# Optimization experiments

Measured on AMD Instinct MI355X. Metric: run time of the kernel, lower is better.

The kernel has to match this reference:

```python
import jax, jax.numpy as jnp
import numpy as np

DIM = 384
DIM_HEAD = 32
HEADS = DIM // DIM_HEAD  # 12
WIN = 8
DIM_FF = 1536
FUSED = DIM + DIM + DIM_FF  # 2304


def setup_inputs() -> dict:
    key = jax.random.key(0)
    ks = jax.random.split(key, 8)
    B, H, W = 16, 64, 64
    x = jax.random.normal(ks[0], (B, DIM, H, W), dtype=jnp.float32)
    s = lambda fan_in: 1.0 / np.sqrt(fan_in)
    w_fused = jax.random.normal(ks[1], (FUSED, DIM), dtype=jnp.float32) * s(DIM)
    w_gate = jax.random.normal(ks[2], (HEADS, DIM), dtype=jnp.float32) * s(DIM)
    b_gate = jnp.full((HEADS,), 0.5, dtype=jnp.float32)  # init_constant_(0.5)
    w_attn_out = jax.random.normal(ks[3], (DIM, DIM), dtype=jnp.float32) * s(DIM)
    w_ff_out = jax.random.normal(ks[4], (DIM, DIM_FF), dtype=jnp.float32) * s(DIM_FF)
    # StarReLU learnable scalars (metaformer defaults)
    sr_scale = jnp.asarray(0.8944, dtype=jnp.float32)
    sr_bias = jnp.asarray(-0.4472, dtype=jnp.float32)
    return {"x": x, "w_fused": w_fused, "w_gate": w_gate, "b_gate": b_gate,
            "w_attn_out": w_attn_out, "w_ff_out": w_ff_out,
            "sr_scale": sr_scale, "sr_bias": sr_bias}


def reference(x, w_fused, w_gate, b_gate, w_attn_out, w_ff_out, sr_scale, sr_bias):
    B, C, H, W = x.shape
    p = WIN
    gh, gw = H // p, W // p
    n = p * p
    # b c (h p1) (w p2) -> (b h w) (p1 p2) c
    xw = x.reshape(B, C, gh, p, gw, p).transpose(0, 2, 4, 3, 5, 1).reshape(B * gh * gw, n, C)
    fused = jnp.einsum('bnc,fc->bnf', xw, w_fused)  # [Bw, n, 2304]
    q, kv, x_ff = jnp.split(fused, [DIM, 2 * DIM], axis=-1)
    # b n (h d) -> b h n d
    q = q.reshape(-1, n, HEADS, DIM_HEAD).transpose(0, 2, 1, 3)
    kv = kv.reshape(-1, n, HEADS, DIM_HEAD).transpose(0, 2, 1, 3)
    scale = 1.0 / np.sqrt(DIM_HEAD)
    scores = jnp.einsum('bhnd,bhmd->bhnm', q, kv) * scale
    attn = jax.nn.softmax(scores, axis=-1)
    x_attn = jnp.einsum('bhnm,bhmd->bhnd', attn, kv)  # kv is both key and value
    gate = jnp.einsum('bnc,hc->bnh', xw, w_gate) + b_gate  # [Bw, n, heads]
    x_attn = x_attn * jax.nn.sigmoid(gate.transpose(0, 2, 1)[..., None])
    x_attn = x_attn.transpose(0, 2, 1, 3).reshape(-1, n, DIM)
    ff = sr_scale * jnp.square(jax.nn.relu(x_ff)) + sr_bias  # StarReLU
    out = jnp.einsum('bnc,oc->bno', x_attn, w_attn_out) + jnp.einsum('bnf,of->bno', ff, w_ff_out)
    # (b h w) (p1 p2) c -> b c (h p1) (w p2)
    out = out.reshape(B, gh, gw, p, p, C).transpose(0, 5, 1, 3, 2, 4).reshape(B, C, H, W)
    return out
```

## Files before the change

### kernel.cpp

```cpp
#include <hip/hip_runtime.h>
#include <hip/hip_bf16.h>

typedef __bf16 bf16x8 __attribute__((ext_vector_type(8), may_alias));
typedef float f32x4 __attribute__((ext_vector_type(4), may_alias));
typedef unsigned short ushort_a __attribute__((may_alias));
typedef unsigned int uint_a __attribute__((may_alias));
typedef unsigned short us8 __attribute__((ext_vector_type(8), may_alias));

#define MFMA(a, b, c) __builtin_amdgcn_mfma_f32_16x16x32_bf16(a, b, c, 0, 0, 0)

__device__ __forceinline__ unsigned short f2bf(float f) {
  return __builtin_bit_cast(unsigned short, (__bf16)f);
}
__device__ __forceinline__ float bf2f(unsigned short u) {
  unsigned v = ((unsigned)u) << 16;
  return __builtin_bit_cast(float, v);
}

__device__ __forceinline__ void kbar() {
  __builtin_amdgcn_sched_barrier(0);
  asm volatile("s_waitcnt lgkmcnt(0)" ::: "memory");
  __builtin_amdgcn_sched_barrier(0);
  __builtin_amdgcn_s_barrier();
  __builtin_amdgcn_sched_barrier(0);
}

#define OFF_WG 884736
#define OFF_WAO 933888
#define OFF_WFO 1081344
#define OFF_XG 1671168
#define OFF_FUSED 26836992
#define OFF_GATE 177831936

__global__ __launch_bounds__(256) void prep_weights(
    const float* __restrict__ wf, const float* __restrict__ wg,
    const float* __restrict__ wao, const float* __restrict__ wfo,
    unsigned short* __restrict__ ws) {
  int i = blockIdx.x * 256 + threadIdx.x;
  if (i < 884736) { ws[i] = f2bf(wf[i]); return; }
  int j = i - 884736;
  if (j < 49152) { ws[i] = f2bf(j < 4608 ? wg[j] : 0.0f); return; }
  j -= 49152;
  if (j < 147456) { ws[i] = f2bf(wao[j]); return; }
  j -= 147456;
  if (j < 589824) ws[i] = f2bf(wfo[j]);
}

__global__ __launch_bounds__(256) void k0_gather(const float* __restrict__ x,
                                                 unsigned short* __restrict__ xg) {
  __shared__ __align__(16) char As[49152];
  int tid = threadIdx.x, wi = blockIdx.x;
  int b = wi >> 6, ghi = (wi >> 3) & 7, gwi = wi & 7;
  const float* xb = x + (size_t)b * 1572864 + (ghi * 8) * 64 + gwi * 8;
  for (int it = 0; it < 12; ++it) {
    int idx = it * 256 + tid;
    int c = idx % 384, p1 = idx / 384;
    const float* src = xb + (size_t)c * 4096 + p1 * 64;
    float4 v0 = *(const float4*)src, v1 = *(const float4*)(src + 4);
    float f[8] = {v0.x, v0.y, v0.z, v0.w, v1.x, v1.y, v1.z, v1.w};
#pragma unroll
    for (int jj = 0; jj < 8; ++jj) {
      int row = p1 * 8 + jj;
      int byte = (row * 768 + c * 2) ^ ((row & 7) << 4);
      *(ushort_a*)(As + byte) = f2bf(f[jj]);
    }
  }
  __syncthreads();
  unsigned short* og = xg + (size_t)wi * 24576;
#pragma unroll
  for (int it = 0; it < 12; ++it) {
    int idx = it * 256 + tid;
    int row = idx / 48, c = idx % 48;
    int byte = (row * 768 + c * 16) ^ ((row & 7) << 4);
    *(us8*)(og + (size_t)row * 384 + c * 8) = *(us8*)(As + byte);
  }
}

__global__ __launch_bounds__(512, 4) void k1_gemm(unsigned short* __restrict__ ws,
                                                  const float* __restrict__ srs,
                                                  const float* __restrict__ srb) {
  __shared__ __align__(16) char sm[65536];
  const int tid = threadIdx.x, lane = tid & 63, wave = tid >> 6;
  const int l15 = lane & 15, l4 = lane >> 4;
  const int wr = wave & 3, wc = wave >> 2;
  const int bid = blockIdx.x;
  const int swz = (bid & 7) * 1216 + (bid >> 3);
  const int mb = swz / 19, nb = swz - mb * 19;
  const unsigned short* Ab = ws + OFF_XG + (size_t)mb * 128 * 384;
  const unsigned short* Bb =
      (nb < 18) ? ws + (size_t)nb * 128 * 384 : ws + OFF_WG;
  const int srow = tid >> 3, sc = tid & 7;
  f32x4 of[2][4] = {};
  us8 sA0[2], sB0[2], sA1[2], sB1[2];

#define K1_LOAD(KS, SA, SB)                                                   \
  {                                                                           \
    _Pragma("unroll") for (int r2 = 0; r2 < 2; ++r2) {                        \
      int row = srow + 64 * r2;                                               \
      SA[r2] = *(const us8*)(Ab + (size_t)row * 384 + (KS)*64 + sc * 8);      \
      SB[r2] = *(const us8*)(Bb + (size_t)row * 384 + (KS)*64 + sc * 8);      \
    }                                                                         \
  }
#define K1_WRITE(BUF, SA, SB)                                                 \
  {                                                                           \
    _Pragma("unroll") for (int r2 = 0; r2 < 2; ++r2) {                        \
      int row = srow + 64 * r2;                                               \
      int byte = ((row * 128 + sc * 16) ^ ((row & 7) << 4)) + (BUF);          \
      *(us8*)(sm + byte) = SA[r2];                                            \
      *(us8*)(sm + 32768 + byte) = SB[r2];                                    \
    }                                                                         \
  }
#define K1_COMPUTE(BUF)                                                       \
  {                                                                           \
    _Pragma("unroll") for (int kk = 0; kk < 2; ++kk) {                        \
      bf16x8 af[2], bfr[4];                                                   \
      _Pragma("unroll") for (int mt = 0; mt < 2; ++mt) {                      \
        int row = wr * 32 + mt * 16 + l15;                                    \
        af[mt] = *(const bf16x8*)(sm + (BUF) +                                \
                 ((row * 128 + kk * 64 + l4 * 16) ^ ((row & 7) << 4)));       \
      }                                                                       \
      _Pragma("unroll") for (int nt = 0; nt < 4; ++nt) {                      \
        int row = wc * 64 + nt * 16 + l15;                                    \
        bfr[nt] = *(const bf16x8*)(sm + 32768 + (BUF) +                       \
                  ((row * 128 + kk * 64 + l4 * 16) ^ ((row & 7) << 4)));      \
      }                                                                       \
      _Pragma("unroll") for (int mt = 0; mt < 2; ++mt)                        \
      _Pragma("unroll") for (int nt = 0; nt < 4; ++nt)                        \
          of[mt][nt] = MFMA(af[mt], bfr[nt], of[mt][nt]);                     \
    }                                                                         \
  }

  K1_LOAD(0, sA0, sB0);
  K1_LOAD(1, sA1, sB1);
  K1_WRITE(0, sA0, sB0);
  __syncthreads();
#pragma unroll 1
  for (int kp = 0; kp < 3; ++kp) {
    int ks = kp * 2;
    if (ks + 2 < 6) K1_LOAD(ks + 2, sA0, sB0);
    K1_COMPUTE(0);
    K1_WRITE(16384, sA1, sB1);
    kbar();
    if (ks + 3 < 6) K1_LOAD(ks + 3, sA1, sB1);
    K1_COMPUTE(16384);
    if (ks + 2 < 6) K1_WRITE(0, sA0, sB0);
    kbar();
  }
  const float ssc = srs[0], sbi = srb[0];
  const bool ffreg = (nb >= 6) && (nb < 18);
#pragma unroll
  for (int mt = 0; mt < 2; ++mt)
#pragma unroll
    for (int nt = 0; nt < 4; ++nt)
#pragma unroll
      for (int rr = 0; rr < 4; ++rr) {
        int row = wr * 32 + mt * 16 + l4 * 4 + rr;
        int col = wc * 64 + nt * 16 + l15;
        float v = of[mt][nt][rr];
        if (ffreg) { v = fmaxf(v, 0.0f); v = ssc * v * v + sbi; }
        *(ushort_a*)(sm + ((row * 256 + col * 2) ^ ((row & 7) << 4))) = f2bf(v);
      }
  __syncthreads();
  if (nb < 18) {
    unsigned short* fo = ws + OFF_FUSED + (size_t)mb * 128 * 2304 + nb * 128;
#pragma unroll
    for (int r2 = 0; r2 < 4; ++r2) {
      int idx = r2 * 512 + tid;
      int row = idx >> 4, c = idx & 15;
      int byte = (row * 256 + c * 16) ^ ((row & 7) << 4);
      __builtin_nontemporal_store(*(us8*)(sm + byte),
                                  (us8*)(fo + (size_t)row * 2304 + c * 8));
    }
  } else {
    unsigned short* go = ws + OFF_GATE + (size_t)mb * 128 * 16;
#pragma unroll
    for (int r2 = 0; r2 < 4; ++r2) {
      int idx = r2 * 512 + tid;
      int row = idx >> 4, c = idx & 15;
      if (c < 2) {
        int byte = (row * 256 + c * 16) ^ ((row & 7) << 4);
        __builtin_nontemporal_store(*(us8*)(sm + byte),
                                    (us8*)(go + (size_t)row * 16 + c * 8));
      }
    }
  }
}

__global__ __launch_bounds__(256, 3) void k2_attn(unsigned short* __restrict__ ws,
                                                  const float* __restrict__ bgate) {
  __shared__ __align__(16) char sm[49152];
  const int tid = threadIdx.x, lane = tid & 63, wave = tid >> 6;
  const int l15 = lane & 15, l4 = lane >> 4;
  char* kvT = sm + wave * 12288;
  char* Pb = kvT + 4096;
  const int wi = blockIdx.x;
  const size_t T0 = (size_t)wi * 64;
  unsigned short* fused = ws + OFF_FUSED;
  const unsigned short* gb = ws + OFF_GATE;
  const f32x4 zz = {};
#pragma unroll 1
  for (int hi = 0; hi < 3; ++hi) {
    const int h = wave + hi * 4;
    bf16x8 akv[4], bq[4];
#pragma unroll
    for (int t = 0; t < 4; ++t) {
      akv[t] = *(const bf16x8*)(fused + (T0 + t * 16 + l15) * 2304 + 384 + h * 32 + l4 * 8);
      bq[t] = *(const bf16x8*)(fused + (T0 + t * 16 + l15) * 2304 + h * 32 + l4 * 8);
    }
    f32x4 sfT[4][4];
#pragma unroll
    for (int mt = 0; mt < 4; ++mt)
#pragma unroll
      for (int ni = 0; ni < 4; ++ni) sfT[mt][ni] = MFMA(akv[mt], bq[ni], zz);
#pragma unroll
    for (int mt = 0; mt < 4; ++mt) {
      us8 u = __builtin_bit_cast(us8, akv[mt]);
      int m = mt * 16 + l15;
#pragma unroll
      for (int j = 0; j < 8; ++j) {
        int d = l4 * 8 + j;
        *(ushort_a*)(kvT + ((d * 128 + m * 2) ^ ((d & 7) << 4))) = u[j];
      }
    }
#pragma unroll
    for (int ni = 0; ni < 4; ++ni) {
      float s[16];
#pragma unroll
      for (int mt = 0; mt < 4; ++mt)
#pragma unroll
        for (int rr = 0; rr < 4; ++rr)
          s[mt * 4 + rr] = sfT[mt][ni][rr] * 0.176776695f;
      float mx = s[0];
#pragma unroll
      for (int q2 = 1; q2 < 16; ++q2) mx = fmaxf(mx, s[q2]);
      mx = fmaxf(mx, __shfl_xor(mx, 16, 64));
      mx = fmaxf(mx, __shfl_xor(mx, 32, 64));
      float sum = 0.0f;
#pragma unroll
      for (int q2 = 0; q2 < 16; ++q2) {
        s[q2] = __expf(s[q2] - mx);
        sum += s[q2];
      }
      sum += __shfl_xor(sum, 16, 64);
      sum += __shfl_xor(sum, 32, 64);
      float rs = 1.0f / sum;
      int n = ni * 16 + l15;
      int rowb = n * 128, sw = (n & 7) << 4;
#pragma unroll
      for (int mt = 0; mt < 4; ++mt) {
        int m = mt * 16 + l4 * 4;
        unsigned p0 = (unsigned)f2bf(s[mt * 4 + 0] * rs) |
                      ((unsigned)f2bf(s[mt * 4 + 1] * rs) << 16);
        unsigned p1 = (unsigned)f2bf(s[mt * 4 + 2] * rs) |
                      ((unsigned)f2bf(s[mt * 4 + 3] * rs) << 16);
        *(uint_a*)(Pb + ((rowb + m * 2) ^ sw)) = p0;
        *(uint_a*)(Pb + ((rowb + (m + 2) * 2) ^ sw)) = p1;
      }
    }
    f32x4 xo[4][2] = {};
#pragma unroll
    for (int ks = 0; ks < 2; ++ks) {
      bf16x8 bv[2];
#pragma unroll
      for (int dt = 0; dt < 2; ++dt) {
        int d = dt * 16 + l15;
        bv[dt] = *(const bf16x8*)(kvT + ((d * 128 + ks * 64 + l4 * 16) ^ ((d & 7) << 4)));
      }
#pragma unroll
      for (int nt = 0; nt < 4; ++nt) {
        int n = nt * 16 + l15;
        bf16x8 ap = *(const bf16x8*)(Pb + ((n * 128 + ks * 64 + l4 * 16) ^ ((n & 7) << 4)));
        xo[nt][0] = MFMA(ap, bv[0], xo[nt][0]);
        xo[nt][1] = MFMA(ap, bv[1], xo[nt][1]);
      }
    }
    const float bgh = bgate[h];
#pragma unroll
    for (int nt = 0; nt < 4; ++nt)
#pragma unroll
      for (int rr = 0; rr < 4; ++rr) {
        int n = nt * 16 + l4 * 4 + rr;
        float gv = bf2f(gb[(T0 + n) * 16 + h]) + bgh;
        float sg = 1.0f / (1.0f + __expf(-gv));
#pragma unroll
        for (int dt = 0; dt < 2; ++dt)
          fused[(T0 + n) * 2304 + h * 32 + dt * 16 + l15] =
              f2bf(xo[nt][dt][rr] * sg);
      }
  }
}

__global__ __launch_bounds__(512, 4) void k3_gemm(const unsigned short* __restrict__ ws,
                                                  float* __restrict__ out) {
  __shared__ __align__(16) char sm[65536];
  const int tid = threadIdx.x, lane = tid & 63, wave = tid >> 6;
  const int l15 = lane & 15, l4 = lane >> 4;
  const int wr = wave & 3, wc = wave >> 2;
  const int bid = blockIdx.x;
  const int swz = (bid & 7) * 192 + (bid >> 3);
  const int mb = swz / 3, nB = swz - mb * 3;
  const size_t T0 = (size_t)mb * 128;
  const unsigned short* fA = ws + OFF_FUSED + T0 * 2304;
  const unsigned short* wao = ws + OFF_WAO + (size_t)(nB * 128) * 384;
  const unsigned short* wfo = ws + OFF_WFO + (size_t)(nB * 128) * 1536;
  const int srow = tid >> 3, sc = tid & 7;
  f32x4 of[2][4] = {};
  us8 sA0[2], sB0[2], sA1[2], sB1[2];

#define K3_LOAD(KS, SA, SB)                                                   \
  {                                                                           \
    int ac = (KS) < 6 ? (KS)*64 : 768 + ((KS)-6) * 64;                        \
    _Pragma("unroll") for (int r2 = 0; r2 < 2; ++r2) {                        \
      int row = srow + 64 * r2;                                               \
      SA[r2] = *(const us8*)(fA + (size_t)row * 2304 + ac + sc * 8);          \
      if ((KS) < 6)                                                           \
        SB[r2] = *(const us8*)(wao + (size_t)row * 384 + (KS)*64 + sc * 8);   \
      else                                                                    \
        SB[r2] =                                                              \
            *(const us8*)(wfo + (size_t)row * 1536 + ((KS)-6) * 64 + sc * 8); \
    }                                                                         \
  }
#define K3_WRITE(BUF, SA, SB)                                                 \
  {                                                                           \
    _Pragma("unroll") for (int r2 = 0; r2 < 2; ++r2) {                        \
      int row = srow + 64 * r2;                                               \
      int byte = ((row * 128 + sc * 16) ^ ((row & 7) << 4)) + (BUF);          \
      *(us8*)(sm + byte) = SA[r2];                                            \
      *(us8*)(sm + 32768 + byte) = SB[r2];                                    \
    }                                                                         \
  }
#define K3_COMPUTE(BUF)                                                       \
  {                                                                           \
    _Pragma("unroll") for (int kk = 0; kk < 2; ++kk) {                        \
      bf16x8 af[2], bfr[4];                                                   \
      _Pragma("unroll") for (int mt = 0; mt < 2; ++mt) {                      \
        int row = wr * 32 + mt * 16 + l15;                                    \
        af[mt] = *(const bf16x8*)(sm + (BUF) +                                \
                 ((row * 128 + kk * 64 + l4 * 16) ^ ((row & 7) << 4)));       \
      }                                                                       \
      _Pragma("unroll") for (int nt = 0; nt < 4; ++nt) {                      \
        int row = wc * 64 + nt * 16 + l15;                                    \
        bfr[nt] = *(const bf16x8*)(sm + 32768 + (BUF) +                       \
                  ((row * 128 + kk * 64 + l4 * 16) ^ ((row & 7) << 4)));      \
      }                                                                       \
      _Pragma("unroll") for (int mt = 0; mt < 2; ++mt)                        \
      _Pragma("unroll") for (int nt = 0; nt < 4; ++nt)                        \
          of[mt][nt] = MFMA(af[mt], bfr[nt], of[mt][nt]);                     \
    }                                                                         \
  }

  K3_LOAD(0, sA0, sB0);
  K3_LOAD(1, sA1, sB1);
  K3_WRITE(0, sA0, sB0);
  __syncthreads();
#pragma unroll 1
  for (int kp = 0; kp < 15; ++kp) {
    int ks = kp * 2;
    if (ks + 2 < 30) K3_LOAD(ks + 2, sA0, sB0);
    K3_COMPUTE(0);
    K3_WRITE(16384, sA1, sB1);
    kbar();
    if (ks + 3 < 30) K3_LOAD(ks + 3, sA1, sB1);
    K3_COMPUTE(16384);
    if (ks + 2 < 30) K3_WRITE(0, sA0, sB0);
    kbar();
  }
#pragma unroll
  for (int mt = 0; mt < 2; ++mt) {
    int n0 = wr * 32 + mt * 16 + l4 * 4;
    int T = (int)T0 + n0;
    int wi = T >> 6, n = T & 63;
    int b = wi >> 6, ghi = (wi >> 3) & 7, gwi = wi & 7;
    float* ob = out + (size_t)b * 1572864 + (size_t)(ghi * 8 + (n >> 3)) * 64 +
                gwi * 8 + (n & 7);
#pragma unroll
    for (int nt = 0; nt < 4; ++nt) {
      int c = nB * 128 + wc * 64 + nt * 16 + l15;
      __builtin_nontemporal_store(of[mt][nt], (f32x4*)(ob + (size_t)c * 4096));
    }
  }
}

extern "C" void kernel_launch(void* const* d_in, const int* in_sizes, int n_in,
                              void* d_out, int out_size, void* d_ws, size_t ws_size,
                              hipStream_t stream) {
  const float* x = (const float*)d_in[0];
  const float* wf = (const float*)d_in[1];
  const float* wg = (const float*)d_in[2];
  const float* bg = (const float*)d_in[3];
  const float* wao = (const float*)d_in[4];
  const float* wfo = (const float*)d_in[5];
  const float* srs = (const float*)d_in[6];
  const float* srb = (const float*)d_in[7];
  unsigned short* ws = (unsigned short*)d_ws;

  prep_weights<<<6528, 256, 0, stream>>>(wf, wg, wao, wfo, ws);
  k0_gather<<<1024, 256, 0, stream>>>(x, ws + OFF_XG);
  k1_gemm<<<512 * 19, 512, 0, stream>>>(ws, srs, srb);
  k2_attn<<<1024, 256, 0, stream>>>(ws, bg);
  k3_gemm<<<512 * 3, 512, 0, stream>>>(ws, (float*)d_out);
}
```

Before: 478.4 us.

## Load GEMM A operand directly into registers, staging only B in LDS

In both the projection GEMM and the output GEMM, each wave now loads its A fragments straight from global memory in MFMA register layout, double-buffered in registers. Only the B tile still goes through swizzled LDS. This halves shared memory per block from 64KB to 32KB, which should allow more resident blocks and cuts LDS write and read traffic. The cost is that the two column-waves fetch the same A rows twice from cache, and those row-strided 16-byte loads are less coalesced than the old cooperative tile load.

```diff
diff --git a/kernel.cpp b/kernel.cpp
--- a/kernel.cpp
+++ b/kernel.cpp
@@ -79,7 +79,7 @@
 __global__ __launch_bounds__(512, 4) void k1_gemm(unsigned short* __restrict__ ws,
                                                   const float* __restrict__ srs,
                                                   const float* __restrict__ srb) {
-  __shared__ __align__(16) char sm[65536];
+  __shared__ __align__(16) char sm[32768];
   const int tid = threadIdx.x, lane = tid & 63, wave = tid >> 6;
   const int l15 = lane & 15, l4 = lane >> 4;
   const int wr = wave & 3, wc = wave >> 2;
@@ -90,60 +90,67 @@
   const unsigned short* Bb =
       (nb < 18) ? ws + (size_t)nb * 128 * 384 : ws + OFF_WG;
   const int srow = tid >> 3, sc = tid & 7;
+  const unsigned short* Arow0 = Ab + (size_t)(wr * 32 + l15) * 384 + l4 * 8;
+  const unsigned short* Arow1 = Arow0 + 16 * 384;
   f32x4 of[2][4] = {};
-  us8 sA0[2], sB0[2], sA1[2], sB1[2];
-
-#define K1_LOAD(KS, SA, SB)                                                   \
+  us8 sB0[2], sB1[2];
+  bf16x8 aA[4], aB[4];
+
+#define K1_LOADB(KS, SB)                                                      \
   {                                                                           \
     _Pragma("unroll") for (int r2 = 0; r2 < 2; ++r2) {                        \
       int row = srow + 64 * r2;                                               \
-      SA[r2] = *(const us8*)(Ab + (size_t)row * 384 + (KS)*64 + sc * 8);      \
       SB[r2] = *(const us8*)(Bb + (size_t)row * 384 + (KS)*64 + sc * 8);      \
     }                                                                         \
   }
-#define K1_WRITE(BUF, SA, SB)                                                 \
+#define K1_LOADA(KS, AR)                                                      \
+  {                                                                           \
+    AR[0] = *(const bf16x8*)(Arow0 + (KS)*64);                                \
+    AR[1] = *(const bf16x8*)(Arow0 + (KS)*64 + 32);                           \
+    AR[2] = *(const bf16x8*)(Arow1 + (KS)*64);                                \
+    AR[3] = *(const bf16x8*)(Arow1 + (KS)*64 + 32);                           \
+  }
+#define K1_WRITEB(BUF, SB)                                                    \
   {                                                                           \
     _Pragma("unroll") for (int r2 = 0; r2 < 2; ++r2) {                        \
       int row = srow + 64 * r2;                                               \
       int byte = ((row * 128 + sc * 16) ^ ((row & 7) << 4)) + (BUF);          \
-      *(us8*)(sm + byte) = SA[r2];                                            \
-      *(us8*)(sm + 32768 + byte) = SB[r2];                                    \
-    }                                                                         \
-  }
-#define K1_COMPUTE(BUF)                                                       \
+      *(us8*)(sm + byte) = SB[r2];                                            \
+    }                                                                         \
+  }
+#define K1_COMPUTE(BUF, AR)                                                   \
   {                                                                           \
     _Pragma("unroll") for (int kk = 0; kk < 2; ++kk) {                        \
-      bf16x8 af[2], bfr[4];                                                   \
-      _Pragma("unroll") for (int mt = 0; mt < 2; ++mt) {                      \
-        int row = wr * 32 + mt * 16 + l15;                                    \
-        af[mt] = *(const bf16x8*)(sm + (BUF) +                                \
-                 ((row * 128 + kk * 64 + l4 * 16) ^ ((row & 7) << 4)));       \
+      bf16x8 bfr[4];                                                          \
+      _Pragma("unroll") for (int nt = 0; nt < 4; ++nt) {                      \
+        int row = wc * 64 + nt * 16 + l15;                                    \
+        bfr[nt] = *(const bf16x8*)(sm + (BUF) +                               \
+                  ((row * 128 + kk * 64 + l4 * 16) ^ ((row & 7) << 4)));      \
       }                                                                       \
       _Pragma("unroll") for (int nt = 0; nt < 4; ++nt) {                      \
-        int row = wc * 64 + nt * 16 + l15;                                    \
-        bfr[nt] = *(const bf16x8*)(sm + 32768 + (BUF) +                       \
-                  ((row * 128 + kk * 64 + l4 * 16) ^ ((row & 7) << 4)));      \
+        of[0][nt] = MFMA(AR[kk], bfr[nt], of[0][nt]);                         \
+        of[1][nt] = MFMA(AR[2 + kk], bfr[nt], of[1][nt]);                     \
       }                                                                       \
-      _Pragma("unroll") for (int mt = 0; mt < 2; ++mt)                        \
-      _Pragma("unroll") for (int nt = 0; nt < 4; ++nt)                        \
-          of[mt][nt] = MFMA(af[mt], bfr[nt], of[mt][nt]);                     \
-    }                                                                         \
-  }
-
-  K1_LOAD(0, sA0, sB0);
-  K1_LOAD(1, sA1, sB1);
-  K1_WRITE(0, sA0, sB0);
+    }                                                                         \
+  }
+
+  K1_LOADB(0, sB0);
+  K1_LOADB(1, sB1);
+  K1_LOADA(0, aA);
+  K1_WRITEB(0, sB0);
   __syncthreads();
 #pragma unroll 1
   for (int kp = 0; kp < 3; ++kp) {
     int ks = kp * 2;
-    if (ks + 2 < 6) K1_LOAD(ks + 2, sA0, sB0);
-    K1_COMPUTE(0);
-    K1_WRITE(16384, sA1, sB1);
+    if (ks + 2 < 6) K1_LOADB(ks + 2, sB0);
+    K1_LOADA(ks + 1, aB);
+    K1_COMPUTE(0, aA);
+    K1_WRITEB(16384, sB1);
     kbar();
-    if (ks + 3 < 6) K1_LOAD(ks + 3, sA1, sB1);
-    K1_COMPUTE(16384);
-    if (ks + 2 < 6) K1_WRITE(0, sA0, sB0);
+    if (ks + 3 < 6) K1_LOADB(ks + 3, sB1);
+    if (ks + 2 < 6) K1_LOADA(ks + 2, aA);
+    K1_COMPUTE(16384, aB);
+    if (ks + 2 < 6) K1_WRITEB(0, sB0);
     kbar();
   }
   const float ssc = srs[0], sbi = srb[0];
@@ -292,7 +299,7 @@
 
 __global__ __launch_bounds__(512, 4) void k3_gemm(const unsigned short* __restrict__ ws,
                                                   float* __restrict__ out) {
-  __shared__ __align__(16) char sm[65536];
+  __shared__ __align__(16) char sm[32768];
   const int tid = threadIdx.x, lane = tid & 63, wave = tid >> 6;
   const int l15 = lane & 15, l4 = lane >> 4;
   const int wr = wave & 3, wc = wave >> 2;
@@ -304,15 +311,16 @@
   const unsigned short* wao = ws + OFF_WAO + (size_t)(nB * 128) * 384;
   const unsigned short* wfo = ws + OFF_WFO + (size_t)(nB * 128) * 1536;
   const int srow = tid >> 3, sc = tid & 7;
+  const unsigned short* Arow0 = fA + (size_t)(wr * 32 + l15) * 2304 + l4 * 8;
+  const unsigned short* Arow1 = Arow0 + 16 * 2304;
   f32x4 of[2][4] = {};
-  us8 sA0[2], sB0[2], sA1[2], sB1[2];
-
-#define K3_LOAD(KS, SA, SB)                                                   \
-  {                                                                           \
-    int ac = (KS) < 6 ? (KS)*64 : 768 + ((KS)-6) * 64;                        \
+  us8 sB0[2], sB1[2];
+  bf16x8 aA[4], aB[4];
+
+#define K3_LOADB(KS, SB)                                                      \
+  {                                                                           \
     _Pragma("unroll") for (int r2 = 0; r2 < 2; ++r2) {                        \
       int row = srow + 64 * r2;                                               \
-      SA[r2] = *(const us8*)(fA + (size_t)row * 2304 + ac + sc * 8);          \
       if ((KS) < 6)                                                           \
         SB[r2] = *(const us8*)(wao + (size_t)row * 384 + (KS)*64 + sc * 8);   \
       else                                                                    \
@@ -320,49 +328,55 @@
             *(const us8*)(wfo + (size_t)row * 1536 + ((KS)-6) * 64 + sc * 8); \
     }                                                                         \
   }
-#define K3_WRITE(BUF, SA, SB)                                                 \
+#define K3_LOADA(KS, AR)                                                      \
+  {                                                                           \
+    int ac = (KS) < 6 ? (KS)*64 : 768 + ((KS)-6) * 64;                        \
+    AR[0] = *(const bf16x8*)(Arow0 + ac);                                     \
+    AR[1] = *(const bf16x8*)(Arow0 + ac + 32);                                \
+    AR[2] = *(const bf16x8*)(Arow1 + ac);                                     \
+    AR[3] = *(const bf16x8*)(Arow1 + ac + 32);                                \
+  }
+#define K3_WRITEB(BUF, SB)                                                    \
   {                                                                           \
     _Pragma("unroll") for (int r2 = 0; r2 < 2; ++r2) {                        \
       int row = srow + 64 * r2;                                               \
       int byte = ((row * 128 + sc * 16) ^ ((row & 7) << 4)) + (BUF);          \
-      *(us8*)(sm + byte) = SA[r2];                                            \
-      *(us8*)(sm + 32768 + byte) = SB[r2];                                    \
-    }                                                                         \
-  }
-#define K3_COMPUTE(BUF)                                                       \
+      *(us8*)(sm + byte) = SB[r2];                                            \
+    }                                                                         \
+  }
+#define K3_COMPUTE(BUF, AR)                                                   \
   {                                                                           \
     _Pragma("unroll") for (int kk = 0; kk < 2; ++kk) {                        \
-      bf16x8 af[2], bfr[4];                                                   \
-      _Pragma("unroll") for (int mt = 0; mt < 2; ++mt) {                      \
-        int row = wr * 32 + mt * 16 + l15;                                    \
-        af[mt] = *(const bf16x8*)(sm + (BUF) +                                \
-                 ((row * 128 + kk * 64 + l4 * 16) ^ ((row & 7) << 4)));       \
+      bf16x8 bfr[4];                                                          \
+      _Pragma("unroll") for (int nt = 0; nt < 4; ++nt) {                      \
+        int row = wc * 64 + nt * 16 + l15;                                    \
+        bfr[nt] = *(const bf16x8*)(sm + (BUF) +                               \
+                  ((row * 128 + kk * 64 + l4 * 16) ^ ((row & 7) << 4)));      \
       }                                                                       \
       _Pragma("unroll") for (int nt = 0; nt < 4; ++nt) {                      \
-        int row = wc * 64 + nt * 16 + l15;                                    \
-        bfr[nt] = *(const bf16x8*)(sm + 32768 + (BUF) +                       \
-                  ((row * 128 + kk * 64 + l4 * 16) ^ ((row & 7) << 4)));      \
+        of[0][nt] = MFMA(AR[kk], bfr[nt], of[0][nt]);                         \
+        of[1][nt] = MFMA(AR[2 + kk], bfr[nt], of[1][nt]);                     \
       }                                                                       \
-      _Pragma("unroll") for (int mt = 0; mt < 2; ++mt)                        \
-      _Pragma("unroll") for (int nt = 0; nt < 4; ++nt)                        \
-          of[mt][nt] = MFMA(af[mt], bfr[nt], of[mt][nt]);                     \
-    }                                                                         \
-  }
-
-  K3_LOAD(0, sA0, sB0);
-  K3_LOAD(1, sA1, sB1);
-  K3_WRITE(0, sA0, sB0);
+    }                                                                         \
+  }
+
+  K3_LOADB(0, sB0);
+  K3_LOADB(1, sB1);
+  K3_LOADA(0, aA);
+  K3_WRITEB(0, sB0);
   __syncthreads();
 #pragma unroll 1
   for (int kp = 0; kp < 15; ++kp) {
     int ks = kp * 2;
-    if (ks + 2 < 30) K3_LOAD(ks + 2, sA0, sB0);
-    K3_COMPUTE(0);
-    K3_WRITE(16384, sA1, sB1);
+    if (ks + 2 < 30) K3_LOADB(ks + 2, sB0);
+    K3_LOADA(ks + 1, aB);
+    K3_COMPUTE(0, aA);
+    K3_WRITEB(16384, sB1);
     kbar();
-    if (ks + 3 < 30) K3_LOAD(ks + 3, sA1, sB1);
-    K3_COMPUTE(16384);
-    if (ks + 2 < 30) K3_WRITE(0, sA0, sB0);
+    if (ks + 3 < 30) K3_LOADB(ks + 3, sB1);
+    if (ks + 2 < 30) K3_LOADA(ks + 2, aA);
+    K3_COMPUTE(16384, aB);
+    if (ks + 2 < 30) K3_WRITEB(0, sB0);
     kbar();
   }
 #pragma unroll
```

Result: slower. 667.5 us (+39.5%).

## Restructure output GEMM to direct global-to-LDS loads with 256-thread blocks

Applied to the files above, without the earlier changes.

The k3 output GEMM drops register-staged double buffering and instead uses global_load_lds to copy A and B tiles straight into a single swizzled LDS buffer. Blocks shrink to 4 waves, each computing a 64x64 subtile, so every wave issues more MFMAs per LDS read. LDS use per block halves, which may allow more resident blocks. The cost is that the single buffer has no overlap between loads and compute, since each k-step waits on a barrier before and after the math.

```diff
diff --git a/kernel.cpp b/kernel.cpp
--- a/kernel.cpp
+++ b/kernel.cpp
@@ -24,6 +24,11 @@
   __builtin_amdgcn_s_barrier();
   __builtin_amdgcn_sched_barrier(0);
 }
+
+#define GLOAD(G, L)                                                          \
+  __builtin_amdgcn_global_load_lds(                                          \
+      (const __attribute__((address_space(1))) unsigned int*)(G),            \
+      (__attribute__((address_space(3))) unsigned int*)(L), 16, 0, 0)
 
 #define OFF_WG 884736
 #define OFF_WAO 933888
@@ -290,12 +295,12 @@
   }
 }
 
-__global__ __launch_bounds__(512, 4) void k3_gemm(const unsigned short* __restrict__ ws,
+__global__ __launch_bounds__(256, 3) void k3_gemm(const unsigned short* __restrict__ ws,
                                                   float* __restrict__ out) {
-  __shared__ __align__(16) char sm[65536];
+  __shared__ __align__(1024) char sm[32768];
   const int tid = threadIdx.x, lane = tid & 63, wave = tid >> 6;
   const int l15 = lane & 15, l4 = lane >> 4;
-  const int wr = wave & 3, wc = wave >> 2;
+  const int wr = wave & 1, wc = wave >> 1;
   const int bid = blockIdx.x;
   const int swz = (bid & 7) * 192 + (bid >> 3);
   const int mb = swz / 3, nB = swz - mb * 3;
@@ -303,71 +308,52 @@
   const unsigned short* fA = ws + OFF_FUSED + T0 * 2304;
   const unsigned short* wao = ws + OFF_WAO + (size_t)(nB * 128) * 384;
   const unsigned short* wfo = ws + OFF_WFO + (size_t)(nB * 128) * 1536;
-  const int srow = tid >> 3, sc = tid & 7;
-  f32x4 of[2][4] = {};
-  us8 sA0[2], sB0[2], sA1[2], sB1[2];
-
-#define K3_LOAD(KS, SA, SB)                                                   \
-  {                                                                           \
-    int ac = (KS) < 6 ? (KS)*64 : 768 + ((KS)-6) * 64;                        \
-    _Pragma("unroll") for (int r2 = 0; r2 < 2; ++r2) {                        \
-      int row = srow + 64 * r2;                                               \
-      SA[r2] = *(const us8*)(fA + (size_t)row * 2304 + ac + sc * 8);          \
-      if ((KS) < 6)                                                           \
-        SB[r2] = *(const us8*)(wao + (size_t)row * 384 + (KS)*64 + sc * 8);   \
-      else                                                                    \
-        SB[r2] =                                                              \
-            *(const us8*)(wfo + (size_t)row * 1536 + ((KS)-6) * 64 + sc * 8); \
-    }                                                                         \
-  }
-#define K3_WRITE(BUF, SA, SB)                                                 \
-  {                                                                           \
-    _Pragma("unroll") for (int r2 = 0; r2 < 2; ++r2) {                        \
-      int row = srow + 64 * r2;                                               \
-      int byte = ((row * 128 + sc * 16) ^ ((row & 7) << 4)) + (BUF);          \
-      *(us8*)(sm + byte) = SA[r2];                                            \
-      *(us8*)(sm + 32768 + byte) = SB[r2];                                    \
-    }                                                                         \
-  }
-#define K3_COMPUTE(BUF)                                                       \
-  {                                                                           \
-    _Pragma("unroll") for (int kk = 0; kk < 2; ++kk) {                        \
-      bf16x8 af[2], bfr[4];                                                   \
-      _Pragma("unroll") for (int mt = 0; mt < 2; ++mt) {                      \
-        int row = wr * 32 + mt * 16 + l15;                                    \
-        af[mt] = *(const bf16x8*)(sm + (BUF) +                                \
-                 ((row * 128 + kk * 64 + l4 * 16) ^ ((row & 7) << 4)));       \
-      }                                                                       \
-      _Pragma("unroll") for (int nt = 0; nt < 4; ++nt) {                      \
-        int row = wc * 64 + nt * 16 + l15;                                    \
-        bfr[nt] = *(const bf16x8*)(sm + 32768 + (BUF) +                       \
-                  ((row * 128 + kk * 64 + l4 * 16) ^ ((row & 7) << 4)));      \
-      }                                                                       \
-      _Pragma("unroll") for (int mt = 0; mt < 2; ++mt)                        \
-      _Pragma("unroll") for (int nt = 0; nt < 4; ++nt)                        \
-          of[mt][nt] = MFMA(af[mt], bfr[nt], of[mt][nt]);                     \
-    }                                                                         \
-  }
-
-  K3_LOAD(0, sA0, sB0);
-  K3_LOAD(1, sA1, sB1);
-  K3_WRITE(0, sA0, sB0);
-  __syncthreads();
+  const int lr = lane >> 3, lc = (lane & 7) ^ lr;
+  const int offA = lr * 2304 + lc * 8;
+  const int offB384 = lr * 384 + lc * 8;
+  const int offB1536 = lr * 1536 + lc * 8;
+  f32x4 of[4][4] = {};
+
 #pragma unroll 1
-  for (int kp = 0; kp < 15; ++kp) {
-    int ks = kp * 2;
-    if (ks + 2 < 30) K3_LOAD(ks + 2, sA0, sB0);
-    K3_COMPUTE(0);
-    K3_WRITE(16384, sA1, sB1);
-    kbar();
-    if (ks + 3 < 30) K3_LOAD(ks + 3, sA1, sB1);
-    K3_COMPUTE(16384);
-    if (ks + 2 < 30) K3_WRITE(0, sA0, sB0);
-    kbar();
-  }
-#pragma unroll
-  for (int mt = 0; mt < 2; ++mt) {
-    int n0 = wr * 32 + mt * 16 + l4 * 4;
+  for (int ks = 0; ks < 30; ++ks) {
+    const int ac = ks < 6 ? ks * 64 : 768 + (ks - 6) * 64;
+#pragma unroll
+    for (int i = 0; i < 4; ++i) {
+      const int R = wave * 32 + i * 8;
+      GLOAD(fA + (size_t)R * 2304 + ac + offA, sm + R * 128);
+      if (ks < 6)
+        GLOAD(wao + (size_t)R * 384 + ks * 64 + offB384, sm + 16384 + R * 128);
+      else
+        GLOAD(wfo + (size_t)R * 1536 + (ks - 6) * 64 + offB1536,
+              sm + 16384 + R * 128);
+    }
+    __syncthreads();
+#pragma unroll
+    for (int kk = 0; kk < 2; ++kk) {
+      bf16x8 af[4], bfr[4];
+#pragma unroll
+      for (int mt = 0; mt < 4; ++mt) {
+        int row = wr * 64 + mt * 16 + l15;
+        af[mt] = *(const bf16x8*)(sm +
+                 ((row * 128 + kk * 64 + l4 * 16) ^ ((row & 7) << 4)));
+      }
+#pragma unroll
+      for (int nt = 0; nt < 4; ++nt) {
+        int row = wc * 64 + nt * 16 + l15;
+        bfr[nt] = *(const bf16x8*)(sm + 16384 +
+                  ((row * 128 + kk * 64 + l4 * 16) ^ ((row & 7) << 4)));
+      }
+#pragma unroll
+      for (int mt = 0; mt < 4; ++mt)
+#pragma unroll
+        for (int nt = 0; nt < 4; ++nt)
+          of[mt][nt] = MFMA(af[mt], bfr[nt], of[mt][nt]);
+    }
+    __syncthreads();
+  }
+#pragma unroll
+  for (int mt = 0; mt < 4; ++mt) {
+    int n0 = wr * 64 + mt * 16 + l4 * 4;
     int T = (int)T0 + n0;
     int wi = T >> 6, n = T & 63;
     int b = wi >> 6, ghi = (wi >> 3) & 7, gwi = wi & 7;
@@ -398,5 +384,5 @@
   k0_gather<<<1024, 256, 0, stream>>>(x, ws + OFF_XG);
   k1_gemm<<<512 * 19, 512, 0, stream>>>(ws, srs, srb);
   k2_attn<<<1024, 256, 0, stream>>>(ws, bg);
-  k3_gemm<<<512 * 3, 512, 0, stream>>>(ws, (float*)d_out);
-}
+  k3_gemm<<<512 * 3, 256, 0, stream>>>(ws, (float*)d_out);
+}
```

After: 476.4 us. About the same (-0.4%).
